# Kernel optimization log

Measured on AMD Instinct MI355X. Metric: run time of the kernel, lower is better.

Reference implementation:

```python
import jax, jax.numpy as jnp
import numpy as np

DIM = 1280
N_HEADS = 10
HEAD_DIM = 128
BASE = 10000.0
BATCH = 2
SEQ = 2048


def _rope(x):
    # x: [b, h, s, d]; matches source: split even/odd channels, rotate, concat halves
    b, h, s, d = x.shape
    theta = 1.0 / (BASE ** (jnp.arange(0, d, 2, dtype=jnp.float32) / d))  # [d/2]
    ang = jnp.arange(s, dtype=jnp.float32)[:, None] * theta               # [s, d/2]
    cos = jnp.cos(ang)
    sin = jnp.sin(ang)
    x1 = x[..., 0::2]
    x2 = x[..., 1::2]
    return jnp.concatenate([x1 * cos - x2 * sin, x1 * sin + x2 * cos], axis=-1)


def setup_inputs() -> dict:
    key = jax.random.key(0)
    ks = jax.random.split(key, 6)
    w_std = 0.02
    x = jax.random.normal(ks[0], (BATCH, SEQ, DIM), dtype=jnp.float32)
    positions = jnp.arange(SEQ, dtype=jnp.int64 if jax.config.jax_enable_x64 else jnp.int32)
    Wq = jax.random.normal(ks[1], (DIM, DIM), dtype=jnp.float32) * w_std
    Wk = jax.random.normal(ks[2], (DIM, DIM), dtype=jnp.float32) * w_std
    Wv = jax.random.normal(ks[3], (DIM, DIM), dtype=jnp.float32) * w_std
    Wo = jax.random.normal(ks[4], (DIM, DIM), dtype=jnp.float32) * w_std
    bq = jnp.zeros((DIM,), jnp.float32)
    bk = jnp.zeros((DIM,), jnp.float32)
    bv = jnp.zeros((DIM,), jnp.float32)
    bo = jnp.zeros((DIM,), jnp.float32)
    return {"x": x, "positions": positions, "Wq": Wq, "bq": bq, "Wk": Wk,
            "bk": bk, "Wv": Wv, "bv": bv, "Wo": Wo, "bo": bo}


def reference(x, positions, Wq, bq, Wk, bk, Wv, bv, Wo, bo):
    b, s, _ = x.shape
    scale = 1.0 / np.sqrt(HEAD_DIM)

    def proj(W, bias):
        y = jnp.einsum('bsd,ed->bse', x, W) + bias  # Linear: x @ W^T + b
        return y.reshape(b, s, N_HEADS, HEAD_DIM).transpose(0, 2, 1, 3)

    q = _rope(proj(Wq, bq))  # [b, h, s, hd]
    k = _rope(proj(Wk, bk))
    v = proj(Wv, bv)

    scores = jnp.einsum('bhqd,bhkd->bhqk', q, k) * scale
    causal = jnp.tril(jnp.ones((s, s), dtype=bool))
    scores = jnp.where(causal, scores, jnp.float32(-jnp.inf))
    attn = jax.nn.softmax(scores, axis=-1)
    out = jnp.einsum('bhqk,bhkd->bhqd', attn, v)
    out = out.transpose(0, 2, 1, 3).reshape(b, s, N_HEADS * HEAD_DIM)
    return jnp.einsum('bse,de->bsd', out, Wo) + bo
```

## Files before the change

### kernel.cpp

```cpp
#include <hip/hip_runtime.h>
#include <cmath>

typedef unsigned short u16;
typedef __attribute__((ext_vector_type(8))) short bf16x8;
typedef __attribute__((ext_vector_type(4))) float f32x4;

#define B_    2
#define SEQ_  2048
#define NH_   10
#define HD_   128
#define DIM_  1280

__device__ __forceinline__ u16 f2bf(float f) {
    union { float f; unsigned u; } v; v.f = f;
    unsigned r = (v.u + 0x7fffu + ((v.u >> 16) & 1u)) >> 16;
    return (u16)r;
}
__device__ __forceinline__ float bf2f(u16 h) {
    union { unsigned u; float f; } v; v.u = ((unsigned)h) << 16;
    return v.f;
}
__device__ __forceinline__ f32x4 mfma16(bf16x8 a, bf16x8 b, f32x4 c) {
    return __builtin_amdgcn_mfma_f32_16x16x32_bf16(a, b, c, 0, 0, 0);
}
__device__ __forceinline__ void g2l16(const void* g, void* l) {
    __builtin_amdgcn_global_load_lds(
        (const __attribute__((address_space(1))) unsigned*)g,
        (__attribute__((address_space(3))) unsigned*)l, 16, 0, 0);
}
__device__ __forceinline__ ushort4 pack4(float a, float b, float c, float d) {
    ushort4 w; w.x = f2bf(a); w.y = f2bf(b); w.z = f2bf(c); w.w = f2bf(d);
    return w;
}
__device__ __forceinline__ bf16x8 ldsr128(unsigned byte_off) {
    bf16x8 r;
    asm volatile("ds_read_b128 %0, %1" : "=v"(r) : "v"(byte_off));
    return r;
}
__device__ __forceinline__ unsigned lds_off(const void* p) {
    return (unsigned)(unsigned long long)
        (__attribute__((address_space(3))) const void*)p;
}

__global__ __launch_bounds__(256) void cvt_k(const float* __restrict__ x,
                                             const float* __restrict__ w0,
                                             const float* __restrict__ w1,
                                             const float* __restrict__ w2,
                                             const float* __restrict__ w3,
                                             u16* __restrict__ xb,
                                             u16* __restrict__ d0,
                                             u16* __restrict__ d1,
                                             u16* __restrict__ d2,
                                             u16* __restrict__ d3,
                                             float* __restrict__ ct,
                                             float* __restrict__ st) {
    const int NX = B_ * SEQ_ * DIM_;
    const int WN = DIM_ * DIM_;
    const int NCV = (NX + 4 * WN) / 8 / 256;
    int bid = blockIdx.x;
    if (bid >= NCV) {
        int idx = (bid - NCV) * 256 + threadIdx.x;
        int s = idx >> 6, j = idx & 63;
        float e = (float)j * (1.0f / 64.0f);
        float theta = 1.0f / powf(10000.0f, e);
        float ang = (float)s * theta;
        ct[idx] = cosf(ang);
        st[idx] = sinf(ang);
        return;
    }
    int i = (bid * 256 + threadIdx.x) * 8;
    const float* src; u16* dst; int off;
    if (i < NX) { src = x; dst = xb; off = i; }
    else {
        int j = i - NX; int w = j / WN; off = j - w * WN;
        src = (w == 0) ? w0 : (w == 1) ? w1 : (w == 2) ? w2 : w3;
        dst = (w == 0) ? d0 : (w == 1) ? d1 : (w == 2) ? d2 : d3;
    }
    float4 a0 = *(const float4*)(src + off);
    float4 a1 = *(const float4*)(src + off + 4);
    union { uint4 q; u16 u[8]; } t;
    t.u[0] = f2bf(a0.x); t.u[1] = f2bf(a0.y);
    t.u[2] = f2bf(a0.z); t.u[3] = f2bf(a0.w);
    t.u[4] = f2bf(a1.x); t.u[5] = f2bf(a1.y);
    t.u[6] = f2bf(a1.z); t.u[7] = f2bf(a1.w);
    *(uint4*)(dst + off) = t.q;
}

template <typename OT>
__device__ __forceinline__ void gemm_core(const u16* __restrict__ A,
                                          const u16* __restrict__ W,
                                          const float* __restrict__ bias,
                                          OT* __restrict__ C,
                                          int m_blk, int n_blk,
                                          u16* As, u16* Bs) {
    const int tid = threadIdx.x;
    const int wave = tid >> 6, lane = tid & 63;
    const int quad = lane >> 4, l16 = lane & 15;
    const int w_m = (wave >> 1) * 64, w_n = (wave & 1) * 64;
    const int srow = wave * 32;
    const int lrow = lane >> 3;
    const int csw = ((lane & 7) ^ lrow) * 8;
    const int rsw = l16 & 7;
    f32x4 acc[4][4] = {};

    const u16* pa = A + (size_t)(m_blk + srow + lrow) * DIM_ + csw;
    const u16* pb = W + (size_t)(n_blk + srow + lrow) * DIM_ + csw;

    for (int k0 = 0; k0 < DIM_; k0 += 64) {
        #pragma unroll
        for (int i = 0; i < 4; ++i) {
            g2l16(pa + k0 + i * 8 * DIM_, As + (srow + i * 8) * 64);
            g2l16(pb + k0 + i * 8 * DIM_, Bs + (srow + i * 8) * 64);
        }
        __syncthreads();
        #pragma unroll
        for (int kk = 0; kk < 2; ++kk) {
            bf16x8 af[4], bf[4];
            #pragma unroll
            for (int mt = 0; mt < 4; ++mt)
                af[mt] = *(const bf16x8*)&As[(w_m + mt * 16 + l16) * 64
                                             + ((kk * 4 + quad) ^ rsw) * 8];
            #pragma unroll
            for (int nt = 0; nt < 4; ++nt)
                bf[nt] = *(const bf16x8*)&Bs[(w_n + nt * 16 + l16) * 64
                                             + ((kk * 4 + quad) ^ rsw) * 8];
            #pragma unroll
            for (int mt = 0; mt < 4; ++mt)
                #pragma unroll
                for (int nt = 0; nt < 4; ++nt)
                    acc[mt][nt] = mfma16(af[mt], bf[nt], acc[mt][nt]);
        }
        __syncthreads();
    }
    #pragma unroll
    for (int nt = 0; nt < 4; ++nt) {
        int col = n_blk + w_n + nt * 16 + l16;
        float bv = bias[col];
        #pragma unroll
        for (int mt = 0; mt < 4; ++mt) {
            #pragma unroll
            for (int r = 0; r < 4; ++r) {
                int row = m_blk + w_m + mt * 16 + quad * 4 + r;
                float v = acc[mt][nt][r] + bv;
                if constexpr (sizeof(OT) == 4) C[(size_t)row * DIM_ + col] = v;
                else C[(size_t)row * DIM_ + col] = (OT)f2bf(v);
            }
        }
    }
}

__device__ __forceinline__ void gemm256_core(const u16* __restrict__ A,
                                             const u16* __restrict__ W,
                                             const float* __restrict__ bias,
                                             u16* __restrict__ C,
                                             int m_blk, int n_blk,
                                             u16* sm) {
    const int tid = threadIdx.x;
    const int wave = tid >> 6, lane = tid & 63;
    const int quad = lane >> 4, l16 = lane & 15;
    const int wr = wave >> 2, wc = wave & 3;
    const int rsw = (l16 >> 1) & 3;
    const unsigned smb = lds_off(sm);
    const unsigned aB = smb + ((wr * 128 + l16) * 32 + (quad ^ rsw) * 8) * 2;
    const unsigned bB = smb + (16384 + (wc * 64 + l16) * 32 + (quad ^ rsw) * 8) * 2;
    const int csw = ((lane & 3) ^ ((lane >> 3) & 3)) * 8;
    const int sdst = wave * 1024;
    const u16* pa = A + (size_t)(m_blk + wave * 32 + (lane >> 2)) * DIM_ + csw;
    const u16* pb = W + (size_t)(n_blk + wave * 32 + (lane >> 2)) * DIM_ + csw;

    f32x4 acc[8][4] = {};

    #pragma unroll
    for (int kk = 0; kk < 2; ++kk) {
        #pragma unroll
        for (int i = 0; i < 2; ++i) {
            g2l16(pa + kk * 32 + i * 16 * DIM_, sm + kk * 8192 + sdst + i * 512);
            g2l16(pb + kk * 32 + i * 16 * DIM_,
                  sm + 16384 + kk * 8192 + sdst + i * 512);
        }
    }
    asm volatile("s_waitcnt vmcnt(4)" ::: "memory");
    __builtin_amdgcn_s_barrier();

    const int NT = DIM_ / 64;
    bf16x8 bf[4];
    for (int t = 0; t < NT; ++t) {
        const int cur = (t & 1) * 32768, nxt = cur ^ 32768;
        const bool st = (t + 1 < NT);
        const u16* pat = pa + (t + 1) * 64;
        const u16* pbt = pb + (t + 1) * 64;
        #pragma unroll
        for (int ph = 0; ph < 4; ++ph) {
            const int kk = ph >> 1, mh = ph & 1;
            if (mh == 0) {
                #pragma unroll
                for (int nt = 0; nt < 4; ++nt)
                    bf[nt] = ldsr128(bB + (cur + kk * 8192 + nt * 512) * 2);
            }
            bf16x8 af[4];
            #pragma unroll
            for (int i = 0; i < 4; ++i)
                af[i] = ldsr128(aB + (cur + kk * 8192 + (mh * 4 + i) * 512) * 2);
            if (st) {
                const u16* ps = (mh == 0) ? pat : pbt;
                #pragma unroll
                for (int i = 0; i < 2; ++i)
                    g2l16(ps + kk * 32 + i * 16 * DIM_,
                          sm + nxt + mh * 16384 + kk * 8192 + sdst + i * 512);
            }
            __builtin_amdgcn_s_barrier();
            asm volatile("s_waitcnt lgkmcnt(0)" ::: "memory");
            __builtin_amdgcn_sched_barrier(0);
            __builtin_amdgcn_s_setprio(1);
            #pragma unroll
            for (int i = 0; i < 4; ++i)
                #pragma unroll
                for (int nt = 0; nt < 4; ++nt)
                    acc[mh * 4 + i][nt] = mfma16(af[i], bf[nt], acc[mh * 4 + i][nt]);
            __builtin_amdgcn_s_setprio(0);
            if (ph & 1) {
                if (st) asm volatile("s_waitcnt vmcnt(4)" ::: "memory");
                else if (ph == 1) asm volatile("s_waitcnt vmcnt(0)" ::: "memory");
            }
            __builtin_amdgcn_s_barrier();
        }
    }
    #pragma unroll
    for (int nt = 0; nt < 4; ++nt) {
        int col = n_blk + wc * 64 + nt * 16 + l16;
        float bv = bias[col];
        #pragma unroll
        for (int mt = 0; mt < 8; ++mt) {
            int row = m_blk + wr * 128 + mt * 16 + quad * 4;
            #pragma unroll
            for (int r = 0; r < 4; ++r)
                C[(size_t)(row + r) * DIM_ + col] = f2bf(acc[mt][nt][r] + bv);
        }
    }
}

__global__ __launch_bounds__(512, 2) void qkv_gemm(const u16* __restrict__ xb,
                                                   const u16* __restrict__ Wqb,
                                                   const u16* __restrict__ Wkb,
                                                   const u16* __restrict__ Wvb,
                                                   const float* __restrict__ bq,
                                                   const float* __restrict__ bk,
                                                   const float* __restrict__ bv,
                                                   u16* __restrict__ Qb,
                                                   u16* __restrict__ Kb,
                                                   u16* __restrict__ Vb) {
    __shared__ alignas(16) u16 sm[65536];
    int id = blockIdx.x;
    int xcd = id & 7, pid = id >> 3;
    int m = xcd * 2 + pid / 15;
    int ns = pid % 15;
    int wsel = ns / 5, n_blk = (ns % 5) * 256;
    const u16* W = (wsel == 0) ? Wqb : (wsel == 1) ? Wkb : Wvb;
    const float* bias = (wsel == 0) ? bq : (wsel == 1) ? bk : bv;
    u16* C = (wsel == 0) ? Qb : (wsel == 1) ? Kb : Vb;
    gemm256_core(xb, W, bias, C, m * 256, n_blk, sm);
}

__global__ __launch_bounds__(256) void out_gemm(const u16* __restrict__ AO,
                                                const u16* __restrict__ Wob,
                                                const float* __restrict__ bo,
                                                float* __restrict__ C) {
    __shared__ alignas(16) u16 As[128 * 64];
    __shared__ alignas(16) u16 Bs[128 * 64];
    int id = blockIdx.x;
    int xcd = id & 7, pid = id >> 3;
    int n = pid % 10;
    int m = xcd * 4 + pid / 10;
    gemm_core<float>(AO, Wob, bo, C, m * 128, n * 128, As, Bs);
}

__global__ __launch_bounds__(256) void rope_k(const u16* __restrict__ Qs_,
                                              const u16* __restrict__ Ks_,
                                              u16* __restrict__ Qd,
                                              u16* __restrict__ Kp,
                                              const float* __restrict__ ct,
                                              const float* __restrict__ st,
                                              float qscale) {
    int t = blockIdx.x * 256 + threadIdx.x;
    const int NR = B_ * SEQ_ * NH_;
    int rid = t >> 3, j0 = (t & 7) * 8;
    const bool isQ = (rid < NR);
    const u16* src = isQ ? Qs_ : Ks_;
    float sc = isQ ? qscale : 1.0f;
    if (!isQ) rid -= NR;
    int h = rid % NH_;
    int s = (rid / NH_) % SEQ_;
    int b = rid / (NH_ * SEQ_);
    const u16* p = src + (size_t)rid * HD_ + 2 * j0;
    union { uint4 q; u16 u[8]; } a0, a1, o1, o2;
    a0.q = *(const uint4*)p;
    a1.q = *(const uint4*)(p + 8);
    const float* cc = ct + (size_t)s * 64 + j0;
    const float* ss = st + (size_t)s * 64 + j0;
    #pragma unroll
    for (int j = 0; j < 8; ++j) {
        float x1 = bf2f((j < 4) ? a0.u[2 * j] : a1.u[2 * j - 8]);
        float x2 = bf2f((j < 4) ? a0.u[2 * j + 1] : a1.u[2 * j - 7]);
        float c = cc[j], sn = ss[j];
        o1.u[j] = f2bf((x1 * c - x2 * sn) * sc);
        o2.u[j] = f2bf((x1 * sn + x2 * c) * sc);
    }
    if (isQ) {
        u16* q = Qd + (size_t)(((size_t)b * SEQ_ + s) * NH_ + h) * HD_;
        *(uint4*)(q + j0) = o1.q;
        *(uint4*)(q + 64 + j0) = o2.q;
    } else {
        int kt = s >> 6, key = s & 63, nt = key >> 4, l16k = key & 15;
        int qd = (j0 >> 3) & 3;
        int kk1 = j0 >> 5, kk2 = 2 + kk1;
        u16* tb = Kp + ((size_t)((b * NH_ + h) * 32 + kt)) * 8192;
        int lane = qd * 16 + l16k;
        *(uint4*)(tb + (kk1 * 4 + nt) * 512 + lane * 8) = o1.q;
        *(uint4*)(tb + (kk2 * 4 + nt) * 512 + lane * 8) = o2.q;
    }
}

__global__ __launch_bounds__(256) void transpose_v(const u16* __restrict__ V,
                                                   u16* __restrict__ Vp) {
    __shared__ u16 T[128][72];
    int stile = blockIdx.x, h = blockIdx.y, b = blockIdx.z;
    int tid = threadIdx.x;
    {
        int sl = tid >> 2, d0 = (tid & 3) * 32;
        const u16* vp = V + ((size_t)((b * SEQ_ + stile * 64 + sl) * NH_ + h)) * HD_ + d0;
        #pragma unroll
        for (int i = 0; i < 4; ++i) {
            union { uint4 q; u16 u[8]; } r;
            r.q = *(const uint4*)(vp + i * 8);
            #pragma unroll
            for (int j = 0; j < 8; ++j) T[d0 + i * 8 + j][sl] = r.u[j];
        }
    }
    __syncthreads();
    {
        int d = tid >> 1, kc = (tid & 1) * 32;
        int dt = d >> 4, l16v = d & 15, kk = kc >> 5;
        u16* tb = Vp + ((size_t)((b * NH_ + h) * 32 + stile)) * 8192 + (kk * 8 + dt) * 512;
        #pragma unroll
        for (int i = 0; i < 4; ++i)
            *(uint4*)(tb + (i * 16 + l16v) * 8) = *(const uint4*)&T[d][kc + i * 8];
    }
}

__device__ const unsigned char QT_TAB[40] =
    {0,1,2,3,4,4,5,5,6,6,7,7,8,8,8,9,9,9,10,10,10,11,11,11,
     12,12,12,12,13,13,13,13,14,14,14,14,15,15,15,15};
__device__ const unsigned char CH_TAB[40] =
    {0,0,0,0,0,1,0,1,0,1,0,1,0,1,2,0,1,2,0,1,2,0,1,2,
     0,1,2,3,0,1,2,3,0,1,2,3,0,1,2,3};

__global__ __launch_bounds__(256, 3) void attn_k(const u16* __restrict__ Q,
                                                 const u16* __restrict__ Kp,
                                                 const u16* __restrict__ Vp,
                                                 u16* __restrict__ AO,
                                                 u16* __restrict__ PO,
                                                 float* __restrict__ Pl) {
    const int cid = blockIdx.x, h = blockIdx.y, b = blockIdx.z;
    const int qt = QT_TAB[cid], c = CH_TAB[cid];
    const int ntiles = 2 * qt + 2;
    const int nch = (ntiles + 7) >> 3;
    const int kt0 = c * 8;
    const int kt1 = (kt0 + 8 < ntiles) ? kt0 + 8 : ntiles;
    const int bh = b * NH_ + h;

    const int tid = threadIdx.x, wave = tid >> 6, lane = tid & 63;
    const int quad = lane >> 4, l16 = lane & 15;

    __shared__ alignas(16) u16 Ks[16 * 512];
    __shared__ alignas(16) u16 Vs[16 * 512];
    __shared__ alignas(16) u16 Pt[4][4][512];

    bf16x8 qf[2][4];
    #pragma unroll
    for (int mt = 0; mt < 2; ++mt) {
        int sq = qt * 128 + wave * 32 + mt * 16 + l16;
        const u16* qp = Q + ((size_t)((b * SEQ_ + sq) * NH_ + h)) * HD_;
        #pragma unroll
        for (int kk = 0; kk < 4; ++kk)
            qf[mt][kk] = *(const bf16x8*)(qp + kk * 32 + quad * 8);
    }
    f32x4 oacc[2][8] = {};
    float l_run[2] = {0.f, 0.f};
    const int q0 = qt * 128 + wave * 32 + l16;

    const u16* kpb = Kp + ((size_t)bh * 32) * 8192;
    const u16* vpb = Vp + ((size_t)bh * 32) * 8192;

    for (int kt = kt0; kt < kt1; ++kt) {
        const u16* kp_t = kpb + (size_t)kt * 8192;
        const u16* vp_t = vpb + (size_t)kt * 8192;
        #pragma unroll
        for (int i = 0; i < 4; ++i) {
            int f = wave * 4 + i;
            g2l16(kp_t + f * 512 + lane * 8, &Ks[f * 512]);
            g2l16(vp_t + f * 512 + lane * 8, &Vs[f * 512]);
        }
        __syncthreads();
        f32x4 sacc[2][4] = {};
        #pragma unroll
        for (int kk = 0; kk < 4; ++kk) {
            #pragma unroll
            for (int nt = 0; nt < 4; ++nt) {
                bf16x8 kf = *(const bf16x8*)&Ks[(kk * 4 + nt) * 512 + lane * 8];
                sacc[0][nt] = mfma16(kf, qf[0][kk], sacc[0][nt]);
                sacc[1][nt] = mfma16(kf, qf[1][kk], sacc[1][nt]);
            }
        }
        const bool maskt = (kt >= 2 * qt);
        const int keyb = kt * 64 + quad * 4;
        #pragma unroll
        for (int mt = 0; mt < 2; ++mt) {
            const int qg = q0 + mt * 16;
            float ps = 0.f;
            #pragma unroll
            for (int nt = 0; nt < 4; ++nt) {
                float p[4];
                #pragma unroll
                for (int r = 0; r < 4; ++r) {
                    float x = sacc[mt][nt][r] - 32.0f;
                    if (maskt && (keyb + nt * 16 + r > qg)) x = -INFINITY;
                    p[r] = __builtin_amdgcn_exp2f(x);
                    ps += p[r];
                }
                ushort4 w4 = pack4(p[0], p[1], p[2], p[3]);
                int rowf = (((nt & 1) << 1) | (quad >> 1)) * 16 + l16;
                *(ushort4*)&Pt[wave][mt * 2 + (nt >> 1)][rowf * 8 + (quad & 1) * 4] = w4;
            }
            l_run[mt] += ps;
        }
        #pragma unroll
        for (int kk = 0; kk < 2; ++kk) {
            bf16x8 pf0 = *(const bf16x8*)&Pt[wave][kk][(quad * 16 + l16) * 8];
            bf16x8 pf1 = *(const bf16x8*)&Pt[wave][2 + kk][(quad * 16 + l16) * 8];
            #pragma unroll
            for (int dt = 0; dt < 8; ++dt) {
                bf16x8 vf = *(const bf16x8*)&Vs[(kk * 8 + dt) * 512 + lane * 8];
                oacc[0][dt] = mfma16(vf, pf0, oacc[0][dt]);
                oacc[1][dt] = mfma16(vf, pf1, oacc[1][dt]);
            }
        }
        __syncthreads();
    }
    #pragma unroll
    for (int mt = 0; mt < 2; ++mt) {
        l_run[mt] += __shfl_xor(l_run[mt], 16, 64);
        l_run[mt] += __shfl_xor(l_run[mt], 32, 64);
    }
    if (nch == 1) {
        #pragma unroll
        for (int mt = 0; mt < 2; ++mt) {
            float invl = 1.0f / l_run[mt];
            int sq = q0 + mt * 16;
            u16* op = AO + ((size_t)((b * SEQ_ + sq) * NH_ + h)) * HD_ + quad * 4;
            #pragma unroll
            for (int dt = 0; dt < 8; ++dt) {
                ushort4 w4 = pack4(oacc[mt][dt][0] * invl, oacc[mt][dt][1] * invl,
                                   oacc[mt][dt][2] * invl, oacc[mt][dt][3] * invl);
                *(ushort4*)(op + dt * 16) = w4;
            }
        }
    } else {
        size_t pidx = ((size_t)bh * 16 + qt) * 4 + c;
        u16* po = PO + pidx * 16384;
        #pragma unroll
        for (int mt = 0; mt < 2; ++mt) {
            #pragma unroll
            for (int dt = 0; dt < 8; ++dt) {
                ushort4 w4 = pack4(oacc[mt][dt][0], oacc[mt][dt][1],
                                   oacc[mt][dt][2], oacc[mt][dt][3]);
                *(ushort4*)(po + ((wave * 16 + mt * 8 + dt) * 64 + lane) * 4) = w4;
            }
            if (quad == 0)
                Pl[pidx * 128 + wave * 32 + mt * 16 + l16] = l_run[mt];
        }
    }
}

__global__ __launch_bounds__(256) void combine_k(const u16* __restrict__ PO,
                                                 const float* __restrict__ Pl,
                                                 u16* __restrict__ AO) {
    const int qt = 4 + blockIdx.x, h = blockIdx.y, b = blockIdx.z;
    const int nch = (2 * qt + 2 + 7) >> 3;
    const int bh = b * NH_ + h;
    const int tid = threadIdx.x;
    const int q = tid >> 1, dh = tid & 1;
    const int wave = q >> 5, mt = (q >> 4) & 1, l16 = q & 15;
    size_t base = ((size_t)bh * 16 + qt) * 4;

    float L = 0.f;
    for (int c = 0; c < nch; ++c) L += Pl[(base + c) * 128 + q];
    float o[64];
    #pragma unroll
    for (int j = 0; j < 64; ++j) o[j] = 0.f;
    for (int c = 0; c < nch; ++c) {
        const u16* p = PO + (base + c) * 16384;
        #pragma unroll
        for (int dtl = 0; dtl < 4; ++dtl) {
            int dt = dh * 4 + dtl;
            #pragma unroll
            for (int quad = 0; quad < 4; ++quad) {
                union { ushort4 v; u16 u[4]; } t;
                t.v = *(const ushort4*)(p + ((wave * 16 + mt * 8 + dt) * 64
                                             + quad * 16 + l16) * 4);
                #pragma unroll
                for (int r = 0; r < 4; ++r)
                    o[dtl * 16 + quad * 4 + r] += bf2f(t.u[r]);
            }
        }
    }
    float invL = 1.0f / L;
    int sq = qt * 128 + q;
    u16* op = AO + ((size_t)((b * SEQ_ + sq) * NH_ + h)) * HD_ + dh * 64;
    union { uint4 v[8]; u16 u[64]; } t;
    #pragma unroll
    for (int j = 0; j < 64; ++j) t.u[j] = f2bf(o[j] * invL);
    #pragma unroll
    for (int i = 0; i < 8; ++i) *(uint4*)(op + i * 8) = t.v[i];
}

extern "C" void kernel_launch(void* const* d_in, const int* in_sizes, int n_in,
                              void* d_out, int out_size, void* d_ws, size_t ws_size,
                              hipStream_t stream) {
    const float* x  = (const float*)d_in[0];
    const float* Wq = (const float*)d_in[2];
    const float* bq = (const float*)d_in[3];
    const float* Wk = (const float*)d_in[4];
    const float* bk = (const float*)d_in[5];
    const float* Wv = (const float*)d_in[6];
    const float* bv = (const float*)d_in[7];
    const float* Wo = (const float*)d_in[8];
    const float* bo = (const float*)d_in[9];
    float* out = (float*)d_out;

    const size_t NE = (size_t)B_ * SEQ_ * NH_ * HD_;
    const size_t WN = (size_t)DIM_ * DIM_;
    u16* Qb  = (u16*)d_ws;
    u16* Kb  = Qb + NE;
    u16* Vb  = Kb + NE;
    u16* Vp  = Vb + NE;
    u16* xb  = Vp + NE;
    u16* Wqb = xb + NE;
    u16* Wkb = Wqb + WN;
    u16* Wvb = Wkb + WN;
    u16* Wob = Wvb + WN;
    float* ct = (float*)(Wob + WN);
    float* st = ct + (size_t)SEQ_ * 64;
    u16* PO  = (u16*)(st + (size_t)SEQ_ * 64);
    float* Pl = (float*)(PO + (size_t)B_ * NH_ * 16 * 4 * 16384);
    u16* Qr = Vb;
    u16* Kp = xb;
    u16* AO = Qb;

    const int NCVT = (B_ * SEQ_ * DIM_ + 4 * (int)WN) / 8 / 256;
    cvt_k<<<NCVT + 512, 256, 0, stream>>>(x, Wq, Wk, Wv, Wo,
                                          xb, Wqb, Wkb, Wvb, Wob, ct, st);

    qkv_gemm<<<dim3(240), 512, 0, stream>>>(xb, Wqb, Wkb, Wvb, bq, bk, bv,
                                            Qb, Kb, Vb);

    transpose_v<<<dim3(SEQ_ / 64, NH_, B_), 256, 0, stream>>>(Vb, Vp);

    const float qsc = 0.08838834764831845f * 1.4426950408889634f;
    rope_k<<<(2 * B_ * SEQ_ * NH_ * 8) / 256, 256, 0, stream>>>(Qb, Kb, Qr, Kp,
                                                                ct, st, qsc);

    attn_k<<<dim3(40, NH_, B_), 256, 0, stream>>>(Qr, Kp, Vp, AO, PO, Pl);
    combine_k<<<dim3(12, NH_, B_), 256, 0, stream>>>(PO, Pl, AO);

    out_gemm<<<dim3(320), 256, 0, stream>>>(AO, Wob, bo, out);
}
```

Measured before the change: 251.4 us.

## Interleave LDS reads with MFMAs and cut barriers in QKV GEMM main loop

Rewrites the 256-tile GEMM k-loop as explicit phases that use graduated lgkmcnt waits, so each row's MFMAs start as soon as its A fragment arrives instead of waiting for every LDS read. The number of workgroup barriers per k-tile drops from eight to two. This is meant to hide LDS latency and reduce synchronization stalls. The risk is hazards on the double-buffered LDS when fewer barriers guard buffer reuse, and the manual waitcnt counts assume the compiler keeps the issue order.

```diff
diff --git a/kernel.cpp b/kernel.cpp
--- a/kernel.cpp
+++ b/kernel.cpp
@@ -41,6 +41,10 @@
     return (unsigned)(unsigned long long)
         (__attribute__((address_space(3))) const void*)p;
 }
+
+#define LGKM(n) do { asm volatile("s_waitcnt lgkmcnt(" #n ")" ::: "memory"); \
+                     __builtin_amdgcn_sched_barrier(0); } while (0)
+#define VMC(n)  asm volatile("s_waitcnt vmcnt(" #n ")" ::: "memory")
 
 __global__ __launch_bounds__(256) void cvt_k(const float* __restrict__ x,
                                              const float* __restrict__ w0,
@@ -149,6 +153,43 @@
     }
 }
 
+#define PHASE(KKE, MH, LOADB, PS, LDD)                                        \
+  {                                                                           \
+    if (LOADB) {                                                              \
+      bf[0] = ldsr128(bC + ((KKE) + 0 * 512) * 2);                            \
+      bf[1] = ldsr128(bC + ((KKE) + 1 * 512) * 2);                            \
+      bf[2] = ldsr128(bC + ((KKE) + 2 * 512) * 2);                            \
+      bf[3] = ldsr128(bC + ((KKE) + 3 * 512) * 2);                            \
+    }                                                                         \
+    bf16x8 af0 = ldsr128(aC + ((KKE) + ((MH) * 4 + 0) * 512) * 2);            \
+    bf16x8 af1 = ldsr128(aC + ((KKE) + ((MH) * 4 + 1) * 512) * 2);            \
+    bf16x8 af2 = ldsr128(aC + ((KKE) + ((MH) * 4 + 2) * 512) * 2);            \
+    bf16x8 af3 = ldsr128(aC + ((KKE) + ((MH) * 4 + 3) * 512) * 2);            \
+    if (st) { g2l16((PS), (LDD)); g2l16((PS) + 16 * DIM_, (LDD) + 512); }     \
+    __builtin_amdgcn_s_setprio(1);                                            \
+    LGKM(3);                                                                  \
+    acc[(MH)*4+0][0] = mfma16(af0, bf[0], acc[(MH)*4+0][0]);                  \
+    acc[(MH)*4+0][1] = mfma16(af0, bf[1], acc[(MH)*4+0][1]);                  \
+    acc[(MH)*4+0][2] = mfma16(af0, bf[2], acc[(MH)*4+0][2]);                  \
+    acc[(MH)*4+0][3] = mfma16(af0, bf[3], acc[(MH)*4+0][3]);                  \
+    LGKM(2);                                                                  \
+    acc[(MH)*4+1][0] = mfma16(af1, bf[0], acc[(MH)*4+1][0]);                  \
+    acc[(MH)*4+1][1] = mfma16(af1, bf[1], acc[(MH)*4+1][1]);                  \
+    acc[(MH)*4+1][2] = mfma16(af1, bf[2], acc[(MH)*4+1][2]);                  \
+    acc[(MH)*4+1][3] = mfma16(af1, bf[3], acc[(MH)*4+1][3]);                  \
+    LGKM(1);                                                                  \
+    acc[(MH)*4+2][0] = mfma16(af2, bf[0], acc[(MH)*4+2][0]);                  \
+    acc[(MH)*4+2][1] = mfma16(af2, bf[1], acc[(MH)*4+2][1]);                  \
+    acc[(MH)*4+2][2] = mfma16(af2, bf[2], acc[(MH)*4+2][2]);                  \
+    acc[(MH)*4+2][3] = mfma16(af2, bf[3], acc[(MH)*4+2][3]);                  \
+    LGKM(0);                                                                  \
+    acc[(MH)*4+3][0] = mfma16(af3, bf[0], acc[(MH)*4+3][0]);                  \
+    acc[(MH)*4+3][1] = mfma16(af3, bf[1], acc[(MH)*4+3][1]);                  \
+    acc[(MH)*4+3][2] = mfma16(af3, bf[2], acc[(MH)*4+3][2]);                  \
+    acc[(MH)*4+3][3] = mfma16(af3, bf[3], acc[(MH)*4+3][3]);                  \
+    __builtin_amdgcn_s_setprio(0);                                            \
+  }
+
 __device__ __forceinline__ void gemm256_core(const u16* __restrict__ A,
                                              const u16* __restrict__ W,
                                              const float* __restrict__ bias,
@@ -179,7 +220,8 @@
                   sm + 16384 + kk * 8192 + sdst + i * 512);
         }
     }
-    asm volatile("s_waitcnt vmcnt(4)" ::: "memory");
+    VMC(4);
+    asm volatile("s_waitcnt lgkmcnt(0)" ::: "memory");
     __builtin_amdgcn_s_barrier();
 
     const int NT = DIM_ / 64;
@@ -187,41 +229,19 @@
     for (int t = 0; t < NT; ++t) {
         const int cur = (t & 1) * 32768, nxt = cur ^ 32768;
         const bool st = (t + 1 < NT);
+        const unsigned aC = aB + cur * 2;
+        const unsigned bC = bB + cur * 2;
         const u16* pat = pa + (t + 1) * 64;
         const u16* pbt = pb + (t + 1) * 64;
-        #pragma unroll
-        for (int ph = 0; ph < 4; ++ph) {
-            const int kk = ph >> 1, mh = ph & 1;
-            if (mh == 0) {
-                #pragma unroll
-                for (int nt = 0; nt < 4; ++nt)
-                    bf[nt] = ldsr128(bB + (cur + kk * 8192 + nt * 512) * 2);
-            }
-            bf16x8 af[4];
-            #pragma unroll
-            for (int i = 0; i < 4; ++i)
-                af[i] = ldsr128(aB + (cur + kk * 8192 + (mh * 4 + i) * 512) * 2);
-            if (st) {
-                const u16* ps = (mh == 0) ? pat : pbt;
-                #pragma unroll
-                for (int i = 0; i < 2; ++i)
-                    g2l16(ps + kk * 32 + i * 16 * DIM_,
-                          sm + nxt + mh * 16384 + kk * 8192 + sdst + i * 512);
-            }
-            __builtin_amdgcn_s_barrier();
-            asm volatile("s_waitcnt lgkmcnt(0)" ::: "memory");
-            __builtin_amdgcn_sched_barrier(0);
-            __builtin_amdgcn_s_setprio(1);
-            #pragma unroll
-            for (int i = 0; i < 4; ++i)
-                #pragma unroll
-                for (int nt = 0; nt < 4; ++nt)
-                    acc[mh * 4 + i][nt] = mfma16(af[i], bf[nt], acc[mh * 4 + i][nt]);
-            __builtin_amdgcn_s_setprio(0);
-            if (ph & 1) {
-                if (st) asm volatile("s_waitcnt vmcnt(4)" ::: "memory");
-                else if (ph == 1) asm volatile("s_waitcnt vmcnt(0)" ::: "memory");
-            }
+
+        PHASE(0, 0, true, pat, sm + nxt + sdst);
+        PHASE(0, 1, false, pbt, sm + nxt + 16384 + sdst);
+        if (st) VMC(4); else VMC(0);
+        __builtin_amdgcn_s_barrier();
+        PHASE(8192, 0, true, pat + 32, sm + nxt + 8192 + sdst);
+        PHASE(8192, 1, false, pbt + 32, sm + nxt + 16384 + 8192 + sdst);
+        if (st) {
+            VMC(4);
             __builtin_amdgcn_s_barrier();
         }
     }
```

Result: faster. 246.1 us (-2.1%).

## Restructure GEMM prefetch to stage B two tiles ahead with per-quarter issue

Applied to the files above, without the earlier changes.

Reworks the 256x256 GEMM main loop so the weight (B) tile is prefetched two k-tiles ahead while the activation (A) tile is prefetched one ahead. The global-to-LDS copies are spread across four phases per k-tile. B fragments for both k-halves are read once per tile, and each phase computes two M-rows over the full 64-wide k. The staging assignment is redistributed so each wave copies one A group and one B group. The aim is to hide global load latency and reduce LDS reads of B. In exchange it uses more registers for the B fragments and needs more delicate waitcnt and buffer-reuse ordering, which risks races.

```diff
diff --git a/kernel.cpp b/kernel.cpp
--- a/kernel.cpp
+++ b/kernel.cpp
@@ -41,6 +41,10 @@
     return (unsigned)(unsigned long long)
         (__attribute__((address_space(3))) const void*)p;
 }
+
+#define LGKM0() do { asm volatile("s_waitcnt lgkmcnt(0)" ::: "memory"); \
+                     __builtin_amdgcn_sched_barrier(0); } while (0)
+#define VMC(n)  asm volatile("s_waitcnt vmcnt(" #n ")" ::: "memory")
 
 __global__ __launch_bounds__(256) void cvt_k(const float* __restrict__ x,
                                              const float* __restrict__ w0,
@@ -164,67 +168,76 @@
     const unsigned aB = smb + ((wr * 128 + l16) * 32 + (quad ^ rsw) * 8) * 2;
     const unsigned bB = smb + (16384 + (wc * 64 + l16) * 32 + (quad ^ rsw) * 8) * 2;
     const int csw = ((lane & 3) ^ ((lane >> 3) & 3)) * 8;
-    const int sdst = wave * 1024;
-    const u16* pa = A + (size_t)(m_blk + wave * 32 + (lane >> 2)) * DIM_ + csw;
-    const u16* pb = W + (size_t)(n_blk + wave * 32 + (lane >> 2)) * DIM_ + csw;
+    const int jA = wave * 2, jB = wave * 2 + 1;
+    const int kkA = jA >> 3, gA0 = jA & 7;
+    const int kkB = jB >> 3, gB0 = jB & 7;
+    const u16* pa = A + (size_t)(m_blk + (lane >> 2)) * DIM_ + csw;
+    const u16* pb = W + (size_t)(n_blk + (lane >> 2)) * DIM_ + csw;
+
+    #define STG(p, mat, d, h, tk) do {                                        \
+        int g0_ = gA0 + (h) * 8, g1_ = gB0 + (h) * 8;                         \
+        g2l16((p) + (size_t)(g0_ * 16) * DIM_ + (tk) * 64 + kkA * 32,         \
+              sm + (d) * 32768 + (mat) * 16384 + kkA * 8192 + g0_ * 512);     \
+        g2l16((p) + (size_t)(g1_ * 16) * DIM_ + (tk) * 64 + kkB * 32,         \
+              sm + (d) * 32768 + (mat) * 16384 + kkB * 8192 + g1_ * 512);     \
+    } while (0)
 
     f32x4 acc[8][4] = {};
-
-    #pragma unroll
-    for (int kk = 0; kk < 2; ++kk) {
-        #pragma unroll
-        for (int i = 0; i < 2; ++i) {
-            g2l16(pa + kk * 32 + i * 16 * DIM_, sm + kk * 8192 + sdst + i * 512);
-            g2l16(pb + kk * 32 + i * 16 * DIM_,
-                  sm + 16384 + kk * 8192 + sdst + i * 512);
-        }
-    }
-    asm volatile("s_waitcnt vmcnt(4)" ::: "memory");
+    bf16x8 b[2][4];
+
+    STG(pa, 0, 0, 0, 0); STG(pa, 0, 0, 1, 0);
+    STG(pb, 1, 0, 0, 0); STG(pb, 1, 0, 1, 0);
+    STG(pb, 1, 1, 0, 1); STG(pb, 1, 1, 1, 1);
+    VMC(4);
+    asm volatile("s_waitcnt lgkmcnt(0)" ::: "memory");
     __builtin_amdgcn_s_barrier();
 
     const int NT = DIM_ / 64;
-    bf16x8 bf[4];
     for (int t = 0; t < NT; ++t) {
-        const int cur = (t & 1) * 32768, nxt = cur ^ 32768;
-        const bool st = (t + 1 < NT);
-        const u16* pat = pa + (t + 1) * 64;
-        const u16* pbt = pb + (t + 1) * 64;
-        #pragma unroll
-        for (int ph = 0; ph < 4; ++ph) {
-            const int kk = ph >> 1, mh = ph & 1;
-            if (mh == 0) {
+        const unsigned cu2 = (unsigned)(t & 1) * 65536u;
+        const int d = t & 1;
+        const bool sa = (t + 1 < NT), sb = (t + 2 < NT);
+        const unsigned aT = aB + cu2, bT = bB + cu2;
+        #pragma unroll
+        for (int q = 0; q < 4; ++q) {
+            if (q == 0) {
                 #pragma unroll
-                for (int nt = 0; nt < 4; ++nt)
-                    bf[nt] = ldsr128(bB + (cur + kk * 8192 + nt * 512) * 2);
-            }
-            bf16x8 af[4];
-            #pragma unroll
-            for (int i = 0; i < 4; ++i)
-                af[i] = ldsr128(aB + (cur + kk * 8192 + (mh * 4 + i) * 512) * 2);
-            if (st) {
-                const u16* ps = (mh == 0) ? pat : pbt;
+                for (int kk = 0; kk < 2; ++kk)
+                    #pragma unroll
+                    for (int nt = 0; nt < 4; ++nt)
+                        b[kk][nt] = ldsr128(bT + (kk * 8192 + nt * 512) * 2);
+            }
+            bf16x8 af[2][2];
+            #pragma unroll
+            for (int j = 0; j < 2; ++j)
                 #pragma unroll
-                for (int i = 0; i < 2; ++i)
-                    g2l16(ps + kk * 32 + i * 16 * DIM_,
-                          sm + nxt + mh * 16384 + kk * 8192 + sdst + i * 512);
-            }
+                for (int kk = 0; kk < 2; ++kk)
+                    af[j][kk] = ldsr128(aT + ((2 * q + j) * 512 + kk * 8192) * 2);
+            if (q == 0 && sa) STG(pa, 0, d ^ 1, 0, t + 1);
+            if (q == 1 && sa) STG(pa, 0, d ^ 1, 1, t + 1);
+            if (q == 2 && sb) STG(pb, 1, d, 0, t + 2);
+            if (q == 3 && sb) STG(pb, 1, d, 1, t + 2);
+            if (q == 0)
+                asm volatile("s_waitcnt lgkmcnt(8)" ::: "memory");
             __builtin_amdgcn_s_barrier();
-            asm volatile("s_waitcnt lgkmcnt(0)" ::: "memory");
-            __builtin_amdgcn_sched_barrier(0);
+            LGKM0();
             __builtin_amdgcn_s_setprio(1);
             #pragma unroll
-            for (int i = 0; i < 4; ++i)
+            for (int j = 0; j < 2; ++j)
                 #pragma unroll
-                for (int nt = 0; nt < 4; ++nt)
-                    acc[mh * 4 + i][nt] = mfma16(af[i], bf[nt], acc[mh * 4 + i][nt]);
+                for (int nt = 0; nt < 4; ++nt) {
+                    acc[2 * q + j][nt] = mfma16(af[j][0], b[0][nt], acc[2 * q + j][nt]);
+                    acc[2 * q + j][nt] = mfma16(af[j][1], b[1][nt], acc[2 * q + j][nt]);
+                }
             __builtin_amdgcn_s_setprio(0);
-            if (ph & 1) {
-                if (st) asm volatile("s_waitcnt vmcnt(4)" ::: "memory");
-                else if (ph == 1) asm volatile("s_waitcnt vmcnt(0)" ::: "memory");
+            if (q == 3) {
+                if (sb) VMC(4);
+                else if (sa) VMC(0);
             }
             __builtin_amdgcn_s_barrier();
         }
     }
+    #undef STG
     #pragma unroll
     for (int nt = 0; nt < 4; ++nt) {
         int col = n_blk + wc * 64 + nt * 16 + l16;
```

After: 248.7 us. Within noise of the previous version (-1.1%).
